# Kernel tuning notes

Hardware: AMD Instinct MI355X
Metric: run time of the kernel (lower is better)

## Reference

```python
import jax, jax.numpy as jnp
import numpy as np

N_ITERS = 20       # fixed iteration count standing in for the tol/max_iters while-loop
ALPHA = 0.1        # self.alpha = -beta with the default beta=-0.1 (assumed from ImplicitLayer)


def setup_inputs() -> dict:
    key = jax.random.key(0)
    ks = jax.random.split(key, 6)
    N, E, F_IN, H, F_OUT = 50000, 800000, 256, 64, 64
    x = jax.random.normal(ks[0], (N, F_IN), dtype=jnp.float32)
    edge_index = jax.random.randint(ks[1], (2, E), 0, N)
    # ~1/avg_degree scaling mimics gcn_norm and keeps the fixed-point iteration stable
    edge_weight = jax.random.uniform(ks[2], (E,), dtype=jnp.float32) * (1.0 / 16.0)
    W_enc = jax.random.normal(ks[3], (F_IN, H), dtype=jnp.float32) / np.sqrt(F_IN).astype(np.float32)
    W_bias = jax.random.normal(ks[4], (H, H), dtype=jnp.float32) / np.sqrt(H).astype(np.float32)
    W_dec = jax.random.normal(ks[5], (H, F_OUT), dtype=jnp.float32) / np.sqrt(H).astype(np.float32)
    return dict(x=x, edge_index=edge_index, edge_weight=edge_weight,
                W_enc=W_enc, W_bias=W_bias, W_dec=W_dec)


def reference(x, edge_index, edge_weight, W_enc, W_bias, W_dec):
    N = x.shape[0]
    src, dst = edge_index[0], edge_index[1]

    h = x @ W_enc                      # encoder, [N, H]; dropout skipped (eval mode)
    b = ALPHA * (h @ W_bias)           # alpha * bias(x): constant across iterations

    def V(u):
        # sparse graph propagation: out[dst] += w * u[src]
        return jax.ops.segment_sum(edge_weight[:, None] * u[src], dst, num_segments=N)

    def step(u, _):
        r = jax.nn.relu(u)                       # nonlin(u)
        u_half = 2.0 * r - u - b
        un = 2.0 * V(u_half) - 2.0 * r + u       # Peaceman-Rachford update
        return un, None

    u, _ = jax.lax.scan(step, jnp.zeros_like(h), None, length=N_ITERS)
    return jax.nn.relu(u) @ W_dec               # act + decoder
```

## Files before the change

kernel.cpp:

```cpp
#include <hip/hip_runtime.h>
#include <hip/hip_fp16.h>

constexpr int H    = 64;
constexpr int FIN  = 256;
constexpr int NIT  = 20;
constexpr int CAP  = 5120;

__device__ __forceinline__ unsigned f2h2(float a, float b) {
    union { unsigned u; __half2 h; } c;
    c.h = __floats2half2_rn(a, b);
    return c.u;
}

__device__ __forceinline__ unsigned short f2hbits(float a) {
    union { __half h; unsigned short us; } c;
    c.h = __float2half_rn(a);
    return c.us;
}

__device__ __forceinline__ float hw(unsigned p) {
    union { unsigned short us; __half h; } c;
    c.us = (unsigned short)(p >> 16);
    return __half2float(c.h);
}

__device__ __forceinline__ void fma4h(const uint2& v, float w, float* acc) {
    union { unsigned u; __half2 h; } c0, c1;
    c0.u = v.x; c1.u = v.y;
    float2 f0 = __half22float2(c0.h), f1 = __half22float2(c1.h);
    acc[0] = fmaf(w, f0.x, acc[0]); acc[1] = fmaf(w, f0.y, acc[1]);
    acc[2] = fmaf(w, f1.x, acc[2]); acc[3] = fmaf(w, f1.y, acc[3]);
}

__device__ __forceinline__ void unpack4(const uint2& v, float* f) {
    union { unsigned u; __half2 h; } c0, c1;
    c0.u = v.x; c1.u = v.y;
    float2 f0 = __half22float2(c0.h), f1 = __half22float2(c1.h);
    f[0] = f0.x; f[1] = f0.y; f[2] = f1.x; f[3] = f1.y;
}

__global__ __launch_bounds__(256) void wc_kernel(const float* __restrict__ We,
                                                 const float* __restrict__ Wb,
                                                 float* __restrict__ Wc) {
    __shared__ float wb[H * H];
    for (int i = threadIdx.x; i < H * H / 4; i += 256)
        reinterpret_cast<float4*>(wb)[i] = reinterpret_cast<const float4*>(Wb)[i];
    __syncthreads();
    int idx = blockIdx.x * 256 + threadIdx.x;
    int i = idx >> 6, j = idx & 63;
    float acc = 0.f;
#pragma unroll 8
    for (int k = 0; k < H; ++k) acc += We[i * H + k] * wb[k * H + j];
    Wc[i * H + j] = acc;
}

__global__ __launch_bounds__(256) void benc_kernel(const float* __restrict__ x,
                                                   const float* __restrict__ Wc,
                                                   unsigned short* __restrict__ bh, int N) {
    __shared__ float xs[64][68];
    __shared__ float wls[64][64];
    const int t  = threadIdx.x;
    const int tr = t >> 4;
    const int tc = t & 15;
    const int n0 = blockIdx.x * 64;

    float4 acc0 = {0,0,0,0}, acc1 = {0,0,0,0}, acc2 = {0,0,0,0}, acc3 = {0,0,0,0};

    for (int kc = 0; kc < FIN; kc += 64) {
        __syncthreads();
        for (int i = t; i < 64 * 64 / 4; i += 256)
            reinterpret_cast<float4*>(&wls[0][0])[i] =
                reinterpret_cast<const float4*>(Wc + (size_t)kc * 64)[i];
        for (int rp = 0; rp < 64; rp += 16) {
            int r = rp + (t & 15);
            int j = t >> 4;
            int c = j * 4;
            int n = n0 + r; if (n >= N) n = N - 1;
            float4 v = reinterpret_cast<const float4*>(x + (size_t)n * FIN + kc)[j];
            xs[c + 0][r] = v.x; xs[c + 1][r] = v.y; xs[c + 2][r] = v.z; xs[c + 3][r] = v.w;
        }
        __syncthreads();
#pragma unroll 8
        for (int k = 0; k < 64; ++k) {
            float4 xv = *reinterpret_cast<const float4*>(&xs[k][tr * 4]);
            float4 wv = *reinterpret_cast<const float4*>(&wls[k][tc * 4]);
            acc0.x = fmaf(xv.x, wv.x, acc0.x); acc0.y = fmaf(xv.x, wv.y, acc0.y);
            acc0.z = fmaf(xv.x, wv.z, acc0.z); acc0.w = fmaf(xv.x, wv.w, acc0.w);
            acc1.x = fmaf(xv.y, wv.x, acc1.x); acc1.y = fmaf(xv.y, wv.y, acc1.y);
            acc1.z = fmaf(xv.y, wv.z, acc1.z); acc1.w = fmaf(xv.y, wv.w, acc1.w);
            acc2.x = fmaf(xv.z, wv.x, acc2.x); acc2.y = fmaf(xv.z, wv.y, acc2.y);
            acc2.z = fmaf(xv.z, wv.z, acc2.z); acc2.w = fmaf(xv.z, wv.w, acc2.w);
            acc3.x = fmaf(xv.w, wv.x, acc3.x); acc3.y = fmaf(xv.w, wv.y, acc3.y);
            acc3.z = fmaf(xv.w, wv.z, acc3.z); acc3.w = fmaf(xv.w, wv.w, acc3.w);
        }
    }
    uint2* bh2 = reinterpret_cast<uint2*>(bh);
    int n;
    n = n0 + tr * 4 + 0;
    if (n < N) bh2[(size_t)n * 16 + tc] =
        make_uint2(f2h2(0.1f*acc0.x, 0.1f*acc0.y), f2h2(0.1f*acc0.z, 0.1f*acc0.w));
    n = n0 + tr * 4 + 1;
    if (n < N) bh2[(size_t)n * 16 + tc] =
        make_uint2(f2h2(0.1f*acc1.x, 0.1f*acc1.y), f2h2(0.1f*acc1.z, 0.1f*acc1.w));
    n = n0 + tr * 4 + 2;
    if (n < N) bh2[(size_t)n * 16 + tc] =
        make_uint2(f2h2(0.1f*acc2.x, 0.1f*acc2.y), f2h2(0.1f*acc2.z, 0.1f*acc2.w));
    n = n0 + tr * 4 + 3;
    if (n < N) bh2[(size_t)n * 16 + tc] =
        make_uint2(f2h2(0.1f*acc3.x, 0.1f*acc3.y), f2h2(0.1f*acc3.z, 0.1f*acc3.w));
}


__global__ void binit_kernel(int* __restrict__ gcur) {
    gcur[threadIdx.x] = threadIdx.x * CAP;
}

constexpr int CHUNK = 4096;
__global__ __launch_bounds__(256) void bucketsct_kernel(const int* __restrict__ ei,
                                                        const float* __restrict__ ew,
                                                        int* __restrict__ gcur,
                                                        unsigned long long* __restrict__ tmp,
                                                        int E) {
    __shared__ int lh[256], lbase[256], lcur[256];
    const int t = threadIdx.x;
    const int e0 = blockIdx.x * CHUNK;
    lh[t] = 0;
    __syncthreads();
    int myd[16], mys[16];
    unsigned short myw[16];
#pragma unroll
    for (int k = 0; k < 16; ++k) {
        int e = e0 + k * 256 + t;
        if (e < E) {
            int d = ei[E + e];
            myd[k] = d; mys[k] = ei[e]; myw[k] = f2hbits(ew[e]);
            atomicAdd(&lh[d >> 8], 1);
        } else myd[k] = -1;
    }
    __syncthreads();
    if (lh[t]) lbase[t] = atomicAdd(&gcur[t], lh[t]);
    lcur[t] = 0;
    __syncthreads();
#pragma unroll
    for (int k = 0; k < 16; ++k) {
        if (myd[k] >= 0) {
            int bkt = myd[k] >> 8;
            int slot = atomicAdd(&lcur[bkt], 1);
            unsigned long long v = ((unsigned long long)(unsigned)myd[k] << 32)
                                 | ((unsigned long long)myw[k] << 16)
                                 | (unsigned)(mys[k] & 0xffff);
            tmp[(size_t)lbase[bkt] + slot] = v;
        }
    }
}

__global__ __launch_bounds__(256) void bscan_kernel(const int* __restrict__ gcur,
                                                    int* __restrict__ goff) {
    __shared__ int sd[256];
    int t = threadIdx.x;
    int c = gcur[t] - t * CAP;
    sd[t] = c;
    __syncthreads();
    for (int o = 1; o < 256; o <<= 1) {
        int v = (t >= o) ? sd[t - o] : 0;
        __syncthreads();
        sd[t] += v;
        __syncthreads();
    }
    goff[t] = sd[t] - c;
    if (t == 255) goff[256] = sd[255];
}

__global__ __launch_bounds__(256) void buildcsr_kernel(const unsigned long long* __restrict__ tmp,
                                                       const int* __restrict__ goff,
                                                       int* __restrict__ row_start,
                                                       unsigned* __restrict__ epk,
                                                       int N, int E) {
    __shared__ int cnt[256], sc[256], pos[256];
    const int b = blockIdx.x;
    const int t = threadIdx.x;
    const int lo = goff[b];
    const int num = goff[b + 1] - lo;
    const unsigned long long* tb = tmp + (size_t)b * CAP;
    cnt[t] = 0;
    __syncthreads();
    for (int i = t; i < num; i += 256)
        atomicAdd(&cnt[(int)((tb[i] >> 32) & 0xff)], 1);
    __syncthreads();
    sc[t] = cnt[t];
    __syncthreads();
    for (int o = 1; o < 256; o <<= 1) {
        int v = (t >= o) ? sc[t - o] : 0;
        __syncthreads();
        sc[t] += v;
        __syncthreads();
    }
    int excl = sc[t] - cnt[t];
    pos[t] = excl;
    int dst = b * 256 + t;
    if (dst < N) row_start[dst] = lo + excl;
    if (b == 0 && t == 0) row_start[N] = E;
    __syncthreads();
    for (int i = t; i < num; i += 256) {
        unsigned long long v = tb[i];
        int dl = (int)((v >> 32) & 0xff);
        int p = atomicAdd(&pos[dl], 1);
        epk[lo + p] = (unsigned)(v & 0xffffffffu);
    }
}

__global__ __launch_bounds__(256) void step_kernel(const uint2* __restrict__ gh,
                                                   const uint2* __restrict__ uhr,
                                                   const uint2* __restrict__ bh,
                                                   const int* __restrict__ row_start,
                                                   const unsigned* __restrict__ epk,
                                                   uint2* __restrict__ outh,
                                                   int N, int NBTOT, int is_first, int is_last) {
    const int wid  = threadIdx.x >> 6;
    const int lane = threadIdx.x & 63;
    const int fq   = lane & 15;

    for (int nb = blockIdx.x; nb < NBTOT; nb += gridDim.x) {
        const int node = nb * 16 + wid * 4 + (lane >> 4);
        if (node >= N) continue;
        const size_t r16 = (size_t)node * 16 + fq;

        uint2 bvv = bh[r16];
        uint2 uvv = uhr[r16];

        const int e0 = row_start[node];
        const int e1 = row_start[node + 1];

        float a0[4] = {0,0,0,0}, a1[4] = {0,0,0,0};
        float a2[4] = {0,0,0,0}, a3[4] = {0,0,0,0};

        for (int base = e0; base < e1; base += 16) {
            int idx = base + fq;
            unsigned p = (idx < e1) ? epk[idx] : 0u;
            const int cnt = min(16, e1 - base);
#pragma unroll
            for (int t0 = 0; t0 < 16; t0 += 4) {
                if (t0 >= cnt) break;
                unsigned p0 = __shfl(p, t0 + 0, 16);
                unsigned p1 = __shfl(p, t0 + 1, 16);
                unsigned p2 = __shfl(p, t0 + 2, 16);
                unsigned p3 = __shfl(p, t0 + 3, 16);
                uint2 v0 = gh[(size_t)(p0 & 0xffffu) * 16 + fq];
                uint2 v1 = gh[(size_t)(p1 & 0xffffu) * 16 + fq];
                uint2 v2 = gh[(size_t)(p2 & 0xffffu) * 16 + fq];
                uint2 v3 = gh[(size_t)(p3 & 0xffffu) * 16 + fq];
                fma4h(v0, hw(p0), a0);
                fma4h(v1, hw(p1), a1);
                fma4h(v2, hw(p2), a2);
                fma4h(v3, hw(p3), a3);
            }
        }
        float s[4];
#pragma unroll
        for (int i = 0; i < 4; ++i) s[i] = (a0[i] + a1[i]) + (a2[i] + a3[i]);

        float bf[4];
        unpack4(bvv, bf);
        float un[4];
        if (is_first) {
#pragma unroll
            for (int i = 0; i < 4; ++i) un[i] = -2.f * s[i];
        } else {
            float uhv[4];
            unpack4(uvv, uhv);
#pragma unroll
            for (int i = 0; i < 4; ++i) un[i] = 2.f * s[i] - uhv[i] - bf[i];
        }
        float ov[4];
        if (is_last) {
#pragma unroll
            for (int i = 0; i < 4; ++i) ov[i] = fmaxf(un[i], 0.f);
        } else {
#pragma unroll
            for (int i = 0; i < 4; ++i) ov[i] = fabsf(un[i]) - bf[i];
        }
        outh[r16] = make_uint2(f2h2(ov[0], ov[1]), f2h2(ov[2], ov[3]));
    }
}

__global__ __launch_bounds__(256) void dec_kernel(const uint2* __restrict__ rh2,
                                                  const float* __restrict__ Wd,
                                                  float* __restrict__ out, int N) {
    __shared__ float xs[64][68];
    __shared__ float wls[64][64];
    const int t  = threadIdx.x;
    const int tr = t >> 4;
    const int tc = t & 15;
    const int n0 = blockIdx.x * 64;

    for (int i = t; i < 64 * 64 / 4; i += 256)
        reinterpret_cast<float4*>(&wls[0][0])[i] = reinterpret_cast<const float4*>(Wd)[i];
    for (int rp = 0; rp < 64; rp += 16) {
        int r = rp + (t & 15);
        int j = t >> 4;
        int c = j * 4;
        int n = n0 + r; if (n >= N) n = N - 1;
        uint2 v = rh2[(size_t)n * 16 + j];
        float f[4];
        unpack4(v, f);
#pragma unroll
        for (int i = 0; i < 4; ++i) xs[c + i][r] = f[i];
    }
    __syncthreads();

    float4 acc0 = {0,0,0,0}, acc1 = {0,0,0,0}, acc2 = {0,0,0,0}, acc3 = {0,0,0,0};
#pragma unroll 8
    for (int k = 0; k < 64; ++k) {
        float4 xv = *reinterpret_cast<const float4*>(&xs[k][tr * 4]);
        float4 wv = *reinterpret_cast<const float4*>(&wls[k][tc * 4]);
        acc0.x = fmaf(xv.x, wv.x, acc0.x); acc0.y = fmaf(xv.x, wv.y, acc0.y);
        acc0.z = fmaf(xv.x, wv.z, acc0.z); acc0.w = fmaf(xv.x, wv.w, acc0.w);
        acc1.x = fmaf(xv.y, wv.x, acc1.x); acc1.y = fmaf(xv.y, wv.y, acc1.y);
        acc1.z = fmaf(xv.y, wv.z, acc1.z); acc1.w = fmaf(xv.y, wv.w, acc1.w);
        acc2.x = fmaf(xv.z, wv.x, acc2.x); acc2.y = fmaf(xv.z, wv.y, acc2.y);
        acc2.z = fmaf(xv.z, wv.z, acc2.z); acc2.w = fmaf(xv.z, wv.w, acc2.w);
        acc3.x = fmaf(xv.w, wv.x, acc3.x); acc3.y = fmaf(xv.w, wv.y, acc3.y);
        acc3.z = fmaf(xv.w, wv.z, acc3.z); acc3.w = fmaf(xv.w, wv.w, acc3.w);
    }
    int n;
    n = n0 + tr * 4 + 0;
    if (n < N) reinterpret_cast<float4*>(out + (size_t)n * 64)[tc] = acc0;
    n = n0 + tr * 4 + 1;
    if (n < N) reinterpret_cast<float4*>(out + (size_t)n * 64)[tc] = acc1;
    n = n0 + tr * 4 + 2;
    if (n < N) reinterpret_cast<float4*>(out + (size_t)n * 64)[tc] = acc2;
    n = n0 + tr * 4 + 3;
    if (n < N) reinterpret_cast<float4*>(out + (size_t)n * 64)[tc] = acc3;
}

extern "C" void kernel_launch(void* const* d_in, const int* in_sizes, int n_in,
                              void* d_out, int out_size, void* d_ws, size_t ws_size,
                              hipStream_t stream) {
    const float* x  = (const float*)d_in[0];
    const int*   ei = (const int*)d_in[1];
    const float* ew = (const float*)d_in[2];
    const float* We = (const float*)d_in[3];
    const float* Wb = (const float*)d_in[4];
    const float* Wd = (const float*)d_in[5];
    float* out = (float*)d_out;

    const int N = in_sizes[0] / FIN;
    const int E = in_sizes[2];

    char* ws = (char*)d_ws;
    size_t off = 0;
    auto alloc = [&](size_t bytes) -> void* {
        void* p = ws + off;
        off = (off + bytes + 255) & ~(size_t)255;
        return p;
    };
    const size_t nodef16 = (size_t)N * H * sizeof(unsigned short);
    unsigned short* bh   = (unsigned short*)alloc(nodef16);
    unsigned short* uhha = (unsigned short*)alloc(nodef16);
    unsigned short* uhhb = (unsigned short*)alloc(nodef16);
    float* Wc   = (float*)alloc((size_t)FIN * H * sizeof(float));
    int*   rsrt = (int*)alloc((size_t)(N + 1) * sizeof(int));
    int*   goff = (int*)alloc(257 * sizeof(int));
    int*   gcur = (int*)alloc(256 * sizeof(int));
    unsigned long long* tmp = (unsigned long long*)alloc((size_t)256 * CAP * sizeof(unsigned long long));
    unsigned* epk = (unsigned*)alloc((size_t)E * sizeof(unsigned));

    binit_kernel<<<1, 256, 0, stream>>>(gcur);
    bucketsct_kernel<<<(E + CHUNK - 1) / CHUNK, 256, 0, stream>>>(ei, ew, gcur, tmp, E);
    bscan_kernel<<<1, 256, 0, stream>>>(gcur, goff);
    const int nbk = (N + 255) >> 8;
    buildcsr_kernel<<<nbk, 256, 0, stream>>>(tmp, goff, rsrt, epk, N, E);

    wc_kernel<<<FIN * H / 256, 256, 0, stream>>>(We, Wb, Wc);
    benc_kernel<<<(N + 63) / 64, 256, 0, stream>>>(x, Wc, bh, N);

    const int NBTOT = (N + 15) / 16;
    const int sgrid = (NBTOT + 1) / 2;
    step_kernel<<<sgrid, 256, 0, stream>>>((const uint2*)bh, (const uint2*)bh, (const uint2*)bh,
                                           rsrt, epk, (uint2*)uhha, N, NBTOT, 1, 0);
    unsigned short *uhcur = uhha, *uhnext = uhhb;
    for (int it = 1; it < NIT; ++it) {
        int last = (it == NIT - 1) ? 1 : 0;
        step_kernel<<<sgrid, 256, 0, stream>>>((const uint2*)uhcur, (const uint2*)uhcur,
                                               (const uint2*)bh, rsrt, epk,
                                               (uint2*)uhnext, N, NBTOT, 0, last);
        unsigned short* th;
        th = uhcur; uhcur = uhnext; uhnext = th;
    }

    dec_kernel<<<(N + 63) / 64, 256, 0, stream>>>((const uint2*)uhcur, Wd, out, N);
}
```

Baseline: 428.0 us.

## Sort nodes by degree for balanced SpMM and fully unroll edge gather

Adds a degree histogram, scan and scatter pass that builds a permutation grouping nodes by in-degree. Each 16-lane group in the step kernel then handles a node from that permutation, so the four nodes in a wavefront have similar edge counts and less divergence. The edge loop now always issues all 16 gathers per chunk using padded index 0 with weight 0, which raises memory-level parallelism. The grid is also changed from a grid-stride loop to one node group per slot. In exchange it adds three small preprocessing kernels and spends gathers on padding edges, and writes from permuted nodes are no longer contiguous.

```diff
diff --git a/kernel.cpp b/kernel.cpp
--- a/kernel.cpp
+++ b/kernel.cpp
@@ -111,8 +111,9 @@
 }
 
 
-__global__ void binit_kernel(int* __restrict__ gcur) {
+__global__ void binit_kernel(int* __restrict__ gcur, int* __restrict__ dh) {
     gcur[threadIdx.x] = threadIdx.x * CAP;
+    if (threadIdx.x < 64) dh[threadIdx.x] = 0;
 }
 
 constexpr int CHUNK = 4096;
@@ -209,78 +210,125 @@
     }
 }
 
+__global__ __launch_bounds__(256) void dhist_kernel(const int* __restrict__ rs,
+                                                    int* __restrict__ dh, int N) {
+    __shared__ int lh[64];
+    if (threadIdx.x < 64) lh[threadIdx.x] = 0;
+    __syncthreads();
+    int n = blockIdx.x * 256 + threadIdx.x;
+    if (n < N) atomicAdd(&lh[min(rs[n + 1] - rs[n], 63)], 1);
+    __syncthreads();
+    if (threadIdx.x < 64 && lh[threadIdx.x]) atomicAdd(&dh[threadIdx.x], lh[threadIdx.x]);
+}
+
+__global__ void dscan_kernel(const int* __restrict__ dh, int* __restrict__ dcur) {
+    int lane = threadIdx.x;
+    int c = dh[lane];
+    int v = c;
+    for (int o = 1; o < 64; o <<= 1) {
+        int t = __shfl_up(v, o);
+        if (lane >= o) v += t;
+    }
+    dcur[lane] = v - c;
+}
+
+__global__ __launch_bounds__(256) void dscatter_kernel(const int* __restrict__ rs,
+                                                       int* __restrict__ dcur,
+                                                       int* __restrict__ perm, int N) {
+    int n = blockIdx.x * 256 + threadIdx.x;
+    if (n < N) {
+        int d = min(rs[n + 1] - rs[n], 63);
+        int pos = atomicAdd(&dcur[d], 1);
+        perm[pos] = n;
+    }
+}
+
 __global__ __launch_bounds__(256) void step_kernel(const uint2* __restrict__ gh,
                                                    const uint2* __restrict__ uhr,
                                                    const uint2* __restrict__ bh,
                                                    const int* __restrict__ row_start,
                                                    const unsigned* __restrict__ epk,
+                                                   const int* __restrict__ perm,
                                                    uint2* __restrict__ outh,
-                                                   int N, int NBTOT, int is_first, int is_last) {
+                                                   int N, int is_first, int is_last) {
     const int wid  = threadIdx.x >> 6;
     const int lane = threadIdx.x & 63;
     const int fq   = lane & 15;
-
-    for (int nb = blockIdx.x; nb < NBTOT; nb += gridDim.x) {
-        const int node = nb * 16 + wid * 4 + (lane >> 4);
-        if (node >= N) continue;
-        const size_t r16 = (size_t)node * 16 + fq;
-
-        uint2 bvv = bh[r16];
-        uint2 uvv = uhr[r16];
-
-        const int e0 = row_start[node];
-        const int e1 = row_start[node + 1];
-
-        float a0[4] = {0,0,0,0}, a1[4] = {0,0,0,0};
-        float a2[4] = {0,0,0,0}, a3[4] = {0,0,0,0};
-
-        for (int base = e0; base < e1; base += 16) {
-            int idx = base + fq;
-            unsigned p = (idx < e1) ? epk[idx] : 0u;
-            const int cnt = min(16, e1 - base);
-#pragma unroll
-            for (int t0 = 0; t0 < 16; t0 += 4) {
-                if (t0 >= cnt) break;
-                unsigned p0 = __shfl(p, t0 + 0, 16);
-                unsigned p1 = __shfl(p, t0 + 1, 16);
-                unsigned p2 = __shfl(p, t0 + 2, 16);
-                unsigned p3 = __shfl(p, t0 + 3, 16);
-                uint2 v0 = gh[(size_t)(p0 & 0xffffu) * 16 + fq];
-                uint2 v1 = gh[(size_t)(p1 & 0xffffu) * 16 + fq];
-                uint2 v2 = gh[(size_t)(p2 & 0xffffu) * 16 + fq];
-                uint2 v3 = gh[(size_t)(p3 & 0xffffu) * 16 + fq];
-                fma4h(v0, hw(p0), a0);
-                fma4h(v1, hw(p1), a1);
-                fma4h(v2, hw(p2), a2);
-                fma4h(v3, hw(p3), a3);
-            }
-        }
-        float s[4];
-#pragma unroll
-        for (int i = 0; i < 4; ++i) s[i] = (a0[i] + a1[i]) + (a2[i] + a3[i]);
-
-        float bf[4];
-        unpack4(bvv, bf);
-        float un[4];
-        if (is_first) {
-#pragma unroll
-            for (int i = 0; i < 4; ++i) un[i] = -2.f * s[i];
-        } else {
-            float uhv[4];
-            unpack4(uvv, uhv);
-#pragma unroll
-            for (int i = 0; i < 4; ++i) un[i] = 2.f * s[i] - uhv[i] - bf[i];
-        }
-        float ov[4];
-        if (is_last) {
-#pragma unroll
-            for (int i = 0; i < 4; ++i) ov[i] = fmaxf(un[i], 0.f);
-        } else {
-#pragma unroll
-            for (int i = 0; i < 4; ++i) ov[i] = fabsf(un[i]) - bf[i];
-        }
-        outh[r16] = make_uint2(f2h2(ov[0], ov[1]), f2h2(ov[2], ov[3]));
-    }
+    const int gid  = (blockIdx.x * 4 + wid) * 4 + (lane >> 4);
+    if (gid >= N) return;
+    const int node = perm[gid];
+    const size_t r16 = (size_t)node * 16 + fq;
+
+    uint2 bvv = bh[r16];
+    uint2 uvv = uhr[r16];
+
+    const int e0 = row_start[node];
+    const int e1 = row_start[node + 1];
+
+    float a0[4] = {0,0,0,0}, a1[4] = {0,0,0,0};
+    float a2[4] = {0,0,0,0}, a3[4] = {0,0,0,0};
+
+    for (int base = e0; base < e1; base += 16) {
+        int idx = base + fq;
+        unsigned p = (idx < e1) ? epk[idx] : 0u;
+        unsigned q0  = __shfl(p,  0, 16), q1  = __shfl(p,  1, 16);
+        unsigned q2  = __shfl(p,  2, 16), q3  = __shfl(p,  3, 16);
+        unsigned q4  = __shfl(p,  4, 16), q5  = __shfl(p,  5, 16);
+        unsigned q6  = __shfl(p,  6, 16), q7  = __shfl(p,  7, 16);
+        unsigned q8  = __shfl(p,  8, 16), q9  = __shfl(p,  9, 16);
+        unsigned q10 = __shfl(p, 10, 16), q11 = __shfl(p, 11, 16);
+        unsigned q12 = __shfl(p, 12, 16), q13 = __shfl(p, 13, 16);
+        unsigned q14 = __shfl(p, 14, 16), q15 = __shfl(p, 15, 16);
+        uint2 v0  = gh[(size_t)(q0  & 0xffffu) * 16 + fq];
+        uint2 v1  = gh[(size_t)(q1  & 0xffffu) * 16 + fq];
+        uint2 v2  = gh[(size_t)(q2  & 0xffffu) * 16 + fq];
+        uint2 v3  = gh[(size_t)(q3  & 0xffffu) * 16 + fq];
+        uint2 v4  = gh[(size_t)(q4  & 0xffffu) * 16 + fq];
+        uint2 v5  = gh[(size_t)(q5  & 0xffffu) * 16 + fq];
+        uint2 v6  = gh[(size_t)(q6  & 0xffffu) * 16 + fq];
+        uint2 v7  = gh[(size_t)(q7  & 0xffffu) * 16 + fq];
+        uint2 v8  = gh[(size_t)(q8  & 0xffffu) * 16 + fq];
+        uint2 v9  = gh[(size_t)(q9  & 0xffffu) * 16 + fq];
+        uint2 v10 = gh[(size_t)(q10 & 0xffffu) * 16 + fq];
+        uint2 v11 = gh[(size_t)(q11 & 0xffffu) * 16 + fq];
+        uint2 v12 = gh[(size_t)(q12 & 0xffffu) * 16 + fq];
+        uint2 v13 = gh[(size_t)(q13 & 0xffffu) * 16 + fq];
+        uint2 v14 = gh[(size_t)(q14 & 0xffffu) * 16 + fq];
+        uint2 v15 = gh[(size_t)(q15 & 0xffffu) * 16 + fq];
+        fma4h(v0,  hw(q0),  a0); fma4h(v1,  hw(q1),  a1);
+        fma4h(v2,  hw(q2),  a2); fma4h(v3,  hw(q3),  a3);
+        fma4h(v4,  hw(q4),  a0); fma4h(v5,  hw(q5),  a1);
+        fma4h(v6,  hw(q6),  a2); fma4h(v7,  hw(q7),  a3);
+        fma4h(v8,  hw(q8),  a0); fma4h(v9,  hw(q9),  a1);
+        fma4h(v10, hw(q10), a2); fma4h(v11, hw(q11), a3);
+        fma4h(v12, hw(q12), a0); fma4h(v13, hw(q13), a1);
+        fma4h(v14, hw(q14), a2); fma4h(v15, hw(q15), a3);
+    }
+    float s[4];
+#pragma unroll
+    for (int i = 0; i < 4; ++i) s[i] = (a0[i] + a1[i]) + (a2[i] + a3[i]);
+
+    float bf[4];
+    unpack4(bvv, bf);
+    float un[4];
+    if (is_first) {
+#pragma unroll
+        for (int i = 0; i < 4; ++i) un[i] = -2.f * s[i];
+    } else {
+        float uhv[4];
+        unpack4(uvv, uhv);
+#pragma unroll
+        for (int i = 0; i < 4; ++i) un[i] = 2.f * s[i] - uhv[i] - bf[i];
+    }
+    float ov[4];
+    if (is_last) {
+#pragma unroll
+        for (int i = 0; i < 4; ++i) ov[i] = fmaxf(un[i], 0.f);
+    } else {
+#pragma unroll
+        for (int i = 0; i < 4; ++i) ov[i] = fabsf(un[i]) - bf[i];
+    }
+    outh[r16] = make_uint2(f2h2(ov[0], ov[1]), f2h2(ov[2], ov[3]));
 }
 
 __global__ __launch_bounds__(256) void dec_kernel(const uint2* __restrict__ rh2,
@@ -362,28 +410,35 @@
     int*   rsrt = (int*)alloc((size_t)(N + 1) * sizeof(int));
     int*   goff = (int*)alloc(257 * sizeof(int));
     int*   gcur = (int*)alloc(256 * sizeof(int));
+    int*   dh   = (int*)alloc(64 * sizeof(int));
+    int*   dcur = (int*)alloc(64 * sizeof(int));
+    int*   perm = (int*)alloc((size_t)N * sizeof(int));
     unsigned long long* tmp = (unsigned long long*)alloc((size_t)256 * CAP * sizeof(unsigned long long));
     unsigned* epk = (unsigned*)alloc((size_t)E * sizeof(unsigned));
 
-    binit_kernel<<<1, 256, 0, stream>>>(gcur);
+    binit_kernel<<<1, 256, 0, stream>>>(gcur, dh);
     bucketsct_kernel<<<(E + CHUNK - 1) / CHUNK, 256, 0, stream>>>(ei, ew, gcur, tmp, E);
     bscan_kernel<<<1, 256, 0, stream>>>(gcur, goff);
     const int nbk = (N + 255) >> 8;
     buildcsr_kernel<<<nbk, 256, 0, stream>>>(tmp, goff, rsrt, epk, N, E);
 
+    const int nnb = (N + 255) / 256;
+    dhist_kernel<<<nnb, 256, 0, stream>>>(rsrt, dh, N);
+    dscan_kernel<<<1, 64, 0, stream>>>(dh, dcur);
+    dscatter_kernel<<<nnb, 256, 0, stream>>>(rsrt, dcur, perm, N);
+
     wc_kernel<<<FIN * H / 256, 256, 0, stream>>>(We, Wb, Wc);
     benc_kernel<<<(N + 63) / 64, 256, 0, stream>>>(x, Wc, bh, N);
 
-    const int NBTOT = (N + 15) / 16;
-    const int sgrid = (NBTOT + 1) / 2;
+    const int sgrid = (N + 15) / 16;
     step_kernel<<<sgrid, 256, 0, stream>>>((const uint2*)bh, (const uint2*)bh, (const uint2*)bh,
-                                           rsrt, epk, (uint2*)uhha, N, NBTOT, 1, 0);
+                                           rsrt, epk, perm, (uint2*)uhha, N, 1, 0);
     unsigned short *uhcur = uhha, *uhnext = uhhb;
     for (int it = 1; it < NIT; ++it) {
         int last = (it == NIT - 1) ? 1 : 0;
         step_kernel<<<sgrid, 256, 0, stream>>>((const uint2*)uhcur, (const uint2*)uhcur,
-                                               (const uint2*)bh, rsrt, epk,
-                                               (uint2*)uhnext, N, NBTOT, 0, last);
+                                               (const uint2*)bh, rsrt, epk, perm,
+                                               (uint2*)uhnext, N, 0, last);
         unsigned short* th;
         th = uhcur; uhcur = uhnext; uhnext = th;
     }
```

Measured after the change: 552.6 us. 29.1% more time.

## Sort nodes by in-degree to balance SpMM step work across wavefronts

Applied to the files above, without the earlier changes.

Adds a counting sort of nodes by in-degree (histogram, scan, scatter into a permutation) and has each step kernel process nodes in that sorted order, so that the 16-lane groups within a wavefront handle rows of similar length and diverge less. The grid-stride loop is also replaced by one block per 16 nodes. The cost is three extra one-time preprocessing kernels and an indirect permutation lookup per node, and neighbouring output rows are no longer written contiguously, which reduces locality on the u and b row accesses.

```diff
diff --git a/kernel.cpp b/kernel.cpp
--- a/kernel.cpp
+++ b/kernel.cpp
@@ -209,78 +209,134 @@
     }
 }
 
+__global__ __launch_bounds__(256) void dhist_kernel(const int* __restrict__ rs,
+                                                    int* __restrict__ bcnt,
+                                                    int N, int NB) {
+    __shared__ int lh[64];
+    if (threadIdx.x < 64) lh[threadIdx.x] = 0;
+    __syncthreads();
+    int n = blockIdx.x * 256 + threadIdx.x;
+    if (n < N) atomicAdd(&lh[min(rs[n + 1] - rs[n], 63)], 1);
+    __syncthreads();
+    if (threadIdx.x < 64) bcnt[threadIdx.x * NB + blockIdx.x] = lh[threadIdx.x];
+}
+
+__global__ __launch_bounds__(1024) void dscan_kernel(const int* __restrict__ bcnt,
+                                                     int* __restrict__ boff, int M) {
+    __shared__ int part[1024];
+    const int t = threadIdx.x;
+    const int K = (M + 1023) / 1024;
+    const int lo = t * K;
+    int sum = 0;
+    for (int i = 0; i < K; ++i) {
+        int idx = lo + i;
+        if (idx < M) sum += bcnt[idx];
+    }
+    part[t] = sum;
+    __syncthreads();
+    for (int o = 1; o < 1024; o <<= 1) {
+        int v = (t >= o) ? part[t - o] : 0;
+        __syncthreads();
+        part[t] += v;
+        __syncthreads();
+    }
+    int run = part[t] - sum;
+    for (int i = 0; i < K; ++i) {
+        int idx = lo + i;
+        if (idx < M) {
+            int c = bcnt[idx];
+            boff[idx] = run;
+            run += c;
+        }
+    }
+}
+
+__global__ __launch_bounds__(256) void dscatter_kernel(const int* __restrict__ rs,
+                                                       const int* __restrict__ boff,
+                                                       int* __restrict__ perm,
+                                                       int N, int NB) {
+    __shared__ int lcur[64];
+    if (threadIdx.x < 64) lcur[threadIdx.x] = 0;
+    __syncthreads();
+    int n = blockIdx.x * 256 + threadIdx.x;
+    if (n < N) {
+        int d = min(rs[n + 1] - rs[n], 63);
+        int local = atomicAdd(&lcur[d], 1);
+        perm[boff[d * NB + blockIdx.x] + local] = n;
+    }
+}
+
 __global__ __launch_bounds__(256) void step_kernel(const uint2* __restrict__ gh,
                                                    const uint2* __restrict__ uhr,
                                                    const uint2* __restrict__ bh,
                                                    const int* __restrict__ row_start,
                                                    const unsigned* __restrict__ epk,
+                                                   const int* __restrict__ perm,
                                                    uint2* __restrict__ outh,
-                                                   int N, int NBTOT, int is_first, int is_last) {
+                                                   int N, int is_first, int is_last) {
     const int wid  = threadIdx.x >> 6;
     const int lane = threadIdx.x & 63;
     const int fq   = lane & 15;
-
-    for (int nb = blockIdx.x; nb < NBTOT; nb += gridDim.x) {
-        const int node = nb * 16 + wid * 4 + (lane >> 4);
-        if (node >= N) continue;
-        const size_t r16 = (size_t)node * 16 + fq;
-
-        uint2 bvv = bh[r16];
-        uint2 uvv = uhr[r16];
-
-        const int e0 = row_start[node];
-        const int e1 = row_start[node + 1];
-
-        float a0[4] = {0,0,0,0}, a1[4] = {0,0,0,0};
-        float a2[4] = {0,0,0,0}, a3[4] = {0,0,0,0};
-
-        for (int base = e0; base < e1; base += 16) {
-            int idx = base + fq;
-            unsigned p = (idx < e1) ? epk[idx] : 0u;
-            const int cnt = min(16, e1 - base);
-#pragma unroll
-            for (int t0 = 0; t0 < 16; t0 += 4) {
-                if (t0 >= cnt) break;
-                unsigned p0 = __shfl(p, t0 + 0, 16);
-                unsigned p1 = __shfl(p, t0 + 1, 16);
-                unsigned p2 = __shfl(p, t0 + 2, 16);
-                unsigned p3 = __shfl(p, t0 + 3, 16);
-                uint2 v0 = gh[(size_t)(p0 & 0xffffu) * 16 + fq];
-                uint2 v1 = gh[(size_t)(p1 & 0xffffu) * 16 + fq];
-                uint2 v2 = gh[(size_t)(p2 & 0xffffu) * 16 + fq];
-                uint2 v3 = gh[(size_t)(p3 & 0xffffu) * 16 + fq];
-                fma4h(v0, hw(p0), a0);
-                fma4h(v1, hw(p1), a1);
-                fma4h(v2, hw(p2), a2);
-                fma4h(v3, hw(p3), a3);
-            }
+    const int gid  = (blockIdx.x * 4 + wid) * 4 + (lane >> 4);
+    if (gid >= N) return;
+    const int node = perm[gid];
+    const size_t r16 = (size_t)node * 16 + fq;
+
+    uint2 bvv = bh[r16];
+    uint2 uvv = uhr[r16];
+
+    const int e0 = row_start[node];
+    const int e1 = row_start[node + 1];
+
+    float a0[4] = {0,0,0,0}, a1[4] = {0,0,0,0};
+    float a2[4] = {0,0,0,0}, a3[4] = {0,0,0,0};
+
+    for (int base = e0; base < e1; base += 16) {
+        int idx = base + fq;
+        unsigned p = (idx < e1) ? epk[idx] : 0u;
+        const int cnt = min(16, e1 - base);
+#pragma unroll
+        for (int t0 = 0; t0 < 16; t0 += 4) {
+            if (t0 >= cnt) break;
+            unsigned p0 = __shfl(p, t0 + 0, 16);
+            unsigned p1 = __shfl(p, t0 + 1, 16);
+            unsigned p2 = __shfl(p, t0 + 2, 16);
+            unsigned p3 = __shfl(p, t0 + 3, 16);
+            uint2 v0 = gh[(size_t)(p0 & 0xffffu) * 16 + fq];
+            uint2 v1 = gh[(size_t)(p1 & 0xffffu) * 16 + fq];
+            uint2 v2 = gh[(size_t)(p2 & 0xffffu) * 16 + fq];
+            uint2 v3 = gh[(size_t)(p3 & 0xffffu) * 16 + fq];
+            fma4h(v0, hw(p0), a0);
+            fma4h(v1, hw(p1), a1);
+            fma4h(v2, hw(p2), a2);
+            fma4h(v3, hw(p3), a3);
         }
-        float s[4];
-#pragma unroll
-        for (int i = 0; i < 4; ++i) s[i] = (a0[i] + a1[i]) + (a2[i] + a3[i]);
-
-        float bf[4];
-        unpack4(bvv, bf);
-        float un[4];
-        if (is_first) {
-#pragma unroll
-            for (int i = 0; i < 4; ++i) un[i] = -2.f * s[i];
-        } else {
-            float uhv[4];
-            unpack4(uvv, uhv);
-#pragma unroll
-            for (int i = 0; i < 4; ++i) un[i] = 2.f * s[i] - uhv[i] - bf[i];
-        }
-        float ov[4];
-        if (is_last) {
-#pragma unroll
-            for (int i = 0; i < 4; ++i) ov[i] = fmaxf(un[i], 0.f);
-        } else {
-#pragma unroll
-            for (int i = 0; i < 4; ++i) ov[i] = fabsf(un[i]) - bf[i];
-        }
-        outh[r16] = make_uint2(f2h2(ov[0], ov[1]), f2h2(ov[2], ov[3]));
-    }
+    }
+    float s[4];
+#pragma unroll
+    for (int i = 0; i < 4; ++i) s[i] = (a0[i] + a1[i]) + (a2[i] + a3[i]);
+
+    float bf[4];
+    unpack4(bvv, bf);
+    float un[4];
+    if (is_first) {
+#pragma unroll
+        for (int i = 0; i < 4; ++i) un[i] = -2.f * s[i];
+    } else {
+        float uhv[4];
+        unpack4(uvv, uhv);
+#pragma unroll
+        for (int i = 0; i < 4; ++i) un[i] = 2.f * s[i] - uhv[i] - bf[i];
+    }
+    float ov[4];
+    if (is_last) {
+#pragma unroll
+        for (int i = 0; i < 4; ++i) ov[i] = fmaxf(un[i], 0.f);
+    } else {
+#pragma unroll
+        for (int i = 0; i < 4; ++i) ov[i] = fabsf(un[i]) - bf[i];
+    }
+    outh[r16] = make_uint2(f2h2(ov[0], ov[1]), f2h2(ov[2], ov[3]));
 }
 
 __global__ __launch_bounds__(256) void dec_kernel(const uint2* __restrict__ rh2,
@@ -362,6 +418,10 @@
     int*   rsrt = (int*)alloc((size_t)(N + 1) * sizeof(int));
     int*   goff = (int*)alloc(257 * sizeof(int));
     int*   gcur = (int*)alloc(256 * sizeof(int));
+    const int NB = (N + 255) / 256;
+    int*   bcnt = (int*)alloc((size_t)64 * NB * sizeof(int));
+    int*   boff = (int*)alloc((size_t)64 * NB * sizeof(int));
+    int*   perm = (int*)alloc((size_t)N * sizeof(int));
     unsigned long long* tmp = (unsigned long long*)alloc((size_t)256 * CAP * sizeof(unsigned long long));
     unsigned* epk = (unsigned*)alloc((size_t)E * sizeof(unsigned));
 
@@ -371,19 +431,22 @@
     const int nbk = (N + 255) >> 8;
     buildcsr_kernel<<<nbk, 256, 0, stream>>>(tmp, goff, rsrt, epk, N, E);
 
+    dhist_kernel<<<NB, 256, 0, stream>>>(rsrt, bcnt, N, NB);
+    dscan_kernel<<<1, 1024, 0, stream>>>(bcnt, boff, 64 * NB);
+    dscatter_kernel<<<NB, 256, 0, stream>>>(rsrt, boff, perm, N, NB);
+
     wc_kernel<<<FIN * H / 256, 256, 0, stream>>>(We, Wb, Wc);
     benc_kernel<<<(N + 63) / 64, 256, 0, stream>>>(x, Wc, bh, N);
 
-    const int NBTOT = (N + 15) / 16;
-    const int sgrid = (NBTOT + 1) / 2;
+    const int sgrid = (N + 15) / 16;
     step_kernel<<<sgrid, 256, 0, stream>>>((const uint2*)bh, (const uint2*)bh, (const uint2*)bh,
-                                           rsrt, epk, (uint2*)uhha, N, NBTOT, 1, 0);
+                                           rsrt, epk, perm, (uint2*)uhha, N, 1, 0);
     unsigned short *uhcur = uhha, *uhnext = uhhb;
     for (int it = 1; it < NIT; ++it) {
         int last = (it == NIT - 1) ? 1 : 0;
         step_kernel<<<sgrid, 256, 0, stream>>>((const uint2*)uhcur, (const uint2*)uhcur,
-                                               (const uint2*)bh, rsrt, epk,
-                                               (uint2*)uhnext, N, NBTOT, 0, last);
+                                               (const uint2*)bh, rsrt, epk, perm,
+                                               (uint2*)uhnext, N, 0, last);
         unsigned short* th;
         th = uhcur; uhcur = uhnext; uhnext = th;
     }
```

Result: faster. 409.5 us (-4.3%).

## Replace capacity-bucket scatter with count-scan-write CSR build and one-block-per-tile steps

Applied to the files above, without the earlier changes.

The edge bucketing now runs as three passes: per-chunk bucket counts, a single-block exclusive scan over all (bucket, chunk) counts, then a write pass that places each edge at its exact offset. This removes the fixed per-bucket capacity, the global atomics and the padded temporary buffer, and it makes the bucket order deterministic, at the cost of an extra pass over the edge list. The step kernel also drops its grid-stride loop, launching one block per 16-node tile instead of half as many blocks that each loop twice.

```diff
diff --git a/kernel.cpp b/kernel.cpp
--- a/kernel.cpp
+++ b/kernel.cpp
@@ -4,7 +4,7 @@
 constexpr int H    = 64;
 constexpr int FIN  = 256;
 constexpr int NIT  = 20;
-constexpr int CAP  = 5120;
+constexpr int CHUNK = 4096;
 
 __device__ __forceinline__ unsigned f2h2(float a, float b) {
     union { unsigned u; __half2 h; } c;
@@ -110,65 +110,81 @@
         make_uint2(f2h2(0.1f*acc3.x, 0.1f*acc3.y), f2h2(0.1f*acc3.z, 0.1f*acc3.w));
 }
 
-
-__global__ void binit_kernel(int* __restrict__ gcur) {
-    gcur[threadIdx.x] = threadIdx.x * CAP;
-}
-
-constexpr int CHUNK = 4096;
-__global__ __launch_bounds__(256) void bucketsct_kernel(const int* __restrict__ ei,
-                                                        const float* __restrict__ ew,
-                                                        int* __restrict__ gcur,
-                                                        unsigned long long* __restrict__ tmp,
-                                                        int E) {
-    __shared__ int lh[256], lbase[256], lcur[256];
+__global__ __launch_bounds__(256) void ccnt_kernel(const int* __restrict__ ei,
+                                                   int* __restrict__ ccnt,
+                                                   int E, int NCH) {
+    __shared__ int lh[256];
     const int t = threadIdx.x;
+    lh[t] = 0;
+    __syncthreads();
     const int e0 = blockIdx.x * CHUNK;
-    lh[t] = 0;
-    __syncthreads();
-    int myd[16], mys[16];
-    unsigned short myw[16];
+#pragma unroll
+    for (int k = 0; k < 16; ++k) {
+        int e = e0 + k * 256 + t;
+        if (e < E) atomicAdd(&lh[ei[E + e] >> 8], 1);
+    }
+    __syncthreads();
+    ccnt[t * NCH + blockIdx.x] = lh[t];
+}
+
+__global__ __launch_bounds__(1024) void cscan_kernel(const int* __restrict__ ccnt,
+                                                     int* __restrict__ cbase,
+                                                     int* __restrict__ goff,
+                                                     int M, int NCH) {
+    __shared__ int part[1024];
+    const int t = threadIdx.x;
+    const int K = (M + 1023) / 1024;
+    const int lo = t * K;
+    int sum = 0;
+    for (int i = 0; i < K; ++i) {
+        int idx = lo + i;
+        if (idx < M) sum += ccnt[idx];
+    }
+    part[t] = sum;
+    __syncthreads();
+    for (int o = 1; o < 1024; o <<= 1) {
+        int v = (t >= o) ? part[t - o] : 0;
+        __syncthreads();
+        part[t] += v;
+        __syncthreads();
+    }
+    int run = part[t] - sum;
+    for (int i = 0; i < K; ++i) {
+        int idx = lo + i;
+        if (idx < M) {
+            int c = ccnt[idx];
+            cbase[idx] = run;
+            if (idx % NCH == 0) goff[idx / NCH] = run;
+            run += c;
+        }
+    }
+    if (t == 1023) goff[256] = part[1023];
+}
+
+__global__ __launch_bounds__(256) void cwrite_kernel(const int* __restrict__ ei,
+                                                     const float* __restrict__ ew,
+                                                     const int* __restrict__ cbase,
+                                                     unsigned long long* __restrict__ tmp,
+                                                     int E, int NCH) {
+    __shared__ int lcur[256];
+    const int t = threadIdx.x;
+    lcur[t] = 0;
+    __syncthreads();
+    const int chunk = blockIdx.x;
+    const int e0 = chunk * CHUNK;
 #pragma unroll
     for (int k = 0; k < 16; ++k) {
         int e = e0 + k * 256 + t;
         if (e < E) {
             int d = ei[E + e];
-            myd[k] = d; mys[k] = ei[e]; myw[k] = f2hbits(ew[e]);
-            atomicAdd(&lh[d >> 8], 1);
-        } else myd[k] = -1;
-    }
-    __syncthreads();
-    if (lh[t]) lbase[t] = atomicAdd(&gcur[t], lh[t]);
-    lcur[t] = 0;
-    __syncthreads();
-#pragma unroll
-    for (int k = 0; k < 16; ++k) {
-        if (myd[k] >= 0) {
-            int bkt = myd[k] >> 8;
-            int slot = atomicAdd(&lcur[bkt], 1);
-            unsigned long long v = ((unsigned long long)(unsigned)myd[k] << 32)
-                                 | ((unsigned long long)myw[k] << 16)
-                                 | (unsigned)(mys[k] & 0xffff);
-            tmp[(size_t)lbase[bkt] + slot] = v;
+            int bkt = d >> 8;
+            int local = atomicAdd(&lcur[bkt], 1);
+            unsigned long long v = ((unsigned long long)(unsigned)d << 32)
+                                 | ((unsigned long long)f2hbits(ew[e]) << 16)
+                                 | (unsigned)(ei[e] & 0xffff);
+            tmp[(size_t)cbase[bkt * NCH + chunk] + local] = v;
         }
     }
-}
-
-__global__ __launch_bounds__(256) void bscan_kernel(const int* __restrict__ gcur,
-                                                    int* __restrict__ goff) {
-    __shared__ int sd[256];
-    int t = threadIdx.x;
-    int c = gcur[t] - t * CAP;
-    sd[t] = c;
-    __syncthreads();
-    for (int o = 1; o < 256; o <<= 1) {
-        int v = (t >= o) ? sd[t - o] : 0;
-        __syncthreads();
-        sd[t] += v;
-        __syncthreads();
-    }
-    goff[t] = sd[t] - c;
-    if (t == 255) goff[256] = sd[255];
 }
 
 __global__ __launch_bounds__(256) void buildcsr_kernel(const unsigned long long* __restrict__ tmp,
@@ -181,7 +197,7 @@
     const int t = threadIdx.x;
     const int lo = goff[b];
     const int num = goff[b + 1] - lo;
-    const unsigned long long* tb = tmp + (size_t)b * CAP;
+    const unsigned long long* tb = tmp + lo;
     cnt[t] = 0;
     __syncthreads();
     for (int i = t; i < num; i += 256)
@@ -215,72 +231,69 @@
                                                    const int* __restrict__ row_start,
                                                    const unsigned* __restrict__ epk,
                                                    uint2* __restrict__ outh,
-                                                   int N, int NBTOT, int is_first, int is_last) {
+                                                   int N, int is_first, int is_last) {
     const int wid  = threadIdx.x >> 6;
     const int lane = threadIdx.x & 63;
     const int fq   = lane & 15;
-
-    for (int nb = blockIdx.x; nb < NBTOT; nb += gridDim.x) {
-        const int node = nb * 16 + wid * 4 + (lane >> 4);
-        if (node >= N) continue;
-        const size_t r16 = (size_t)node * 16 + fq;
-
-        uint2 bvv = bh[r16];
-        uint2 uvv = uhr[r16];
-
-        const int e0 = row_start[node];
-        const int e1 = row_start[node + 1];
-
-        float a0[4] = {0,0,0,0}, a1[4] = {0,0,0,0};
-        float a2[4] = {0,0,0,0}, a3[4] = {0,0,0,0};
-
-        for (int base = e0; base < e1; base += 16) {
-            int idx = base + fq;
-            unsigned p = (idx < e1) ? epk[idx] : 0u;
-            const int cnt = min(16, e1 - base);
-#pragma unroll
-            for (int t0 = 0; t0 < 16; t0 += 4) {
-                if (t0 >= cnt) break;
-                unsigned p0 = __shfl(p, t0 + 0, 16);
-                unsigned p1 = __shfl(p, t0 + 1, 16);
-                unsigned p2 = __shfl(p, t0 + 2, 16);
-                unsigned p3 = __shfl(p, t0 + 3, 16);
-                uint2 v0 = gh[(size_t)(p0 & 0xffffu) * 16 + fq];
-                uint2 v1 = gh[(size_t)(p1 & 0xffffu) * 16 + fq];
-                uint2 v2 = gh[(size_t)(p2 & 0xffffu) * 16 + fq];
-                uint2 v3 = gh[(size_t)(p3 & 0xffffu) * 16 + fq];
-                fma4h(v0, hw(p0), a0);
-                fma4h(v1, hw(p1), a1);
-                fma4h(v2, hw(p2), a2);
-                fma4h(v3, hw(p3), a3);
-            }
+    const int node = (blockIdx.x * 4 + wid) * 4 + (lane >> 4);
+    if (node >= N) return;
+    const size_t r16 = (size_t)node * 16 + fq;
+
+    uint2 bvv = bh[r16];
+    uint2 uvv = uhr[r16];
+
+    const int e0 = row_start[node];
+    const int e1 = row_start[node + 1];
+
+    float a0[4] = {0,0,0,0}, a1[4] = {0,0,0,0};
+    float a2[4] = {0,0,0,0}, a3[4] = {0,0,0,0};
+
+    for (int base = e0; base < e1; base += 16) {
+        int idx = base + fq;
+        unsigned p = (idx < e1) ? epk[idx] : 0u;
+        const int cnt = min(16, e1 - base);
+#pragma unroll
+        for (int t0 = 0; t0 < 16; t0 += 4) {
+            if (t0 >= cnt) break;
+            unsigned p0 = __shfl(p, t0 + 0, 16);
+            unsigned p1 = __shfl(p, t0 + 1, 16);
+            unsigned p2 = __shfl(p, t0 + 2, 16);
+            unsigned p3 = __shfl(p, t0 + 3, 16);
+            uint2 v0 = gh[(size_t)(p0 & 0xffffu) * 16 + fq];
+            uint2 v1 = gh[(size_t)(p1 & 0xffffu) * 16 + fq];
+            uint2 v2 = gh[(size_t)(p2 & 0xffffu) * 16 + fq];
+            uint2 v3 = gh[(size_t)(p3 & 0xffffu) * 16 + fq];
+            fma4h(v0, hw(p0), a0);
+            fma4h(v1, hw(p1), a1);
+            fma4h(v2, hw(p2), a2);
+            fma4h(v3, hw(p3), a3);
         }
-        float s[4];
-#pragma unroll
-        for (int i = 0; i < 4; ++i) s[i] = (a0[i] + a1[i]) + (a2[i] + a3[i]);
-
-        float bf[4];
-        unpack4(bvv, bf);
-        float un[4];
-        if (is_first) {
-#pragma unroll
-            for (int i = 0; i < 4; ++i) un[i] = -2.f * s[i];
-        } else {
-            float uhv[4];
-            unpack4(uvv, uhv);
-#pragma unroll
-            for (int i = 0; i < 4; ++i) un[i] = 2.f * s[i] - uhv[i] - bf[i];
-        }
-        float ov[4];
-        if (is_last) {
-#pragma unroll
-            for (int i = 0; i < 4; ++i) ov[i] = fmaxf(un[i], 0.f);
-        } else {
-#pragma unroll
-            for (int i = 0; i < 4; ++i) ov[i] = fabsf(un[i]) - bf[i];
-        }
-        outh[r16] = make_uint2(f2h2(ov[0], ov[1]), f2h2(ov[2], ov[3]));
-    }
+    }
+    float s[4];
+#pragma unroll
+    for (int i = 0; i < 4; ++i) s[i] = (a0[i] + a1[i]) + (a2[i] + a3[i]);
+
+    float bf[4];
+    unpack4(bvv, bf);
+    float un[4];
+    if (is_first) {
+#pragma unroll
+        for (int i = 0; i < 4; ++i) un[i] = -2.f * s[i];
+    } else {
+        float uhv[4];
+        unpack4(uvv, uhv);
+#pragma unroll
+        for (int i = 0; i < 4; ++i) un[i] = 2.f * s[i] - uhv[i] - bf[i];
+    }
+    float ov[4];
+    if (is_last) {
+#pragma unroll
+        for (int i = 0; i < 4; ++i) ov[i] = fmaxf(un[i], 0.f);
+    } else {
+#pragma unroll
+        for (int i = 0; i < 4; ++i) ov[i] = fabsf(un[i]) - bf[i];
+    }
+    outh[r16] = make_uint2(f2h2(ov[0], ov[1]), f2h2(ov[2], ov[3]));
 }
 
 __global__ __launch_bounds__(256) void dec_kernel(const uint2* __restrict__ rh2,
@@ -346,6 +359,7 @@
 
     const int N = in_sizes[0] / FIN;
     const int E = in_sizes[2];
+    const int NCH = (E + CHUNK - 1) / CHUNK;
 
     char* ws = (char*)d_ws;
     size_t off = 0;
@@ -361,29 +375,29 @@
     float* Wc   = (float*)alloc((size_t)FIN * H * sizeof(float));
     int*   rsrt = (int*)alloc((size_t)(N + 1) * sizeof(int));
     int*   goff = (int*)alloc(257 * sizeof(int));
-    int*   gcur = (int*)alloc(256 * sizeof(int));
-    unsigned long long* tmp = (unsigned long long*)alloc((size_t)256 * CAP * sizeof(unsigned long long));
+    int*   ccnt = (int*)alloc((size_t)256 * NCH * sizeof(int));
+    int*   cbase= (int*)alloc((size_t)256 * NCH * sizeof(int));
+    unsigned long long* tmp = (unsigned long long*)alloc((size_t)E * sizeof(unsigned long long));
     unsigned* epk = (unsigned*)alloc((size_t)E * sizeof(unsigned));
 
-    binit_kernel<<<1, 256, 0, stream>>>(gcur);
-    bucketsct_kernel<<<(E + CHUNK - 1) / CHUNK, 256, 0, stream>>>(ei, ew, gcur, tmp, E);
-    bscan_kernel<<<1, 256, 0, stream>>>(gcur, goff);
+    ccnt_kernel<<<NCH, 256, 0, stream>>>(ei, ccnt, E, NCH);
+    cscan_kernel<<<1, 1024, 0, stream>>>(ccnt, cbase, goff, 256 * NCH, NCH);
+    cwrite_kernel<<<NCH, 256, 0, stream>>>(ei, ew, cbase, tmp, E, NCH);
     const int nbk = (N + 255) >> 8;
     buildcsr_kernel<<<nbk, 256, 0, stream>>>(tmp, goff, rsrt, epk, N, E);
 
     wc_kernel<<<FIN * H / 256, 256, 0, stream>>>(We, Wb, Wc);
     benc_kernel<<<(N + 63) / 64, 256, 0, stream>>>(x, Wc, bh, N);
 
-    const int NBTOT = (N + 15) / 16;
-    const int sgrid = (NBTOT + 1) / 2;
+    const int sgrid = (N + 15) / 16;
     step_kernel<<<sgrid, 256, 0, stream>>>((const uint2*)bh, (const uint2*)bh, (const uint2*)bh,
-                                           rsrt, epk, (uint2*)uhha, N, NBTOT, 1, 0);
+                                           rsrt, epk, (uint2*)uhha, N, 1, 0);
     unsigned short *uhcur = uhha, *uhnext = uhhb;
     for (int it = 1; it < NIT; ++it) {
         int last = (it == NIT - 1) ? 1 : 0;
         step_kernel<<<sgrid, 256, 0, stream>>>((const uint2*)uhcur, (const uint2*)uhcur,
                                                (const uint2*)bh, rsrt, epk,
-                                               (uint2*)uhnext, N, NBTOT, 0, last);
+                                               (uint2*)uhnext, N, 0, last);
         unsigned short* th;
         th = uhcur; uhcur = uhnext; uhnext = th;
     }
```

Result: slower. 485.9 us (+13.5%).
